# Kernel optimization log

Hardware: AMD Instinct MI355X
Metric: run time of the kernel (lower is better)

Reference implementation:

```python
import jax, jax.numpy as jnp
import numpy as np

N_NODES = 50000


def _gcn_layer(x, src, dst, norm_src, norm_dst, W, b, act):
    # DGL GraphConv with norm='both': D_out^{-1/2} A D_in^{-1/2} X W + b
    h = x * norm_src[:, None]                      # scale by src out-degree
    m = h[src]                                     # gather messages [E, d]
    agg = jax.ops.segment_sum(m, dst, num_segments=N_NODES)  # scatter-add
    agg = agg * norm_dst[:, None]
    out = agg @ W + b
    if act:
        out = jax.nn.relu(out)
    return out


def setup_inputs() -> dict:
    key = jax.random.key(0)
    ks = jax.random.split(key, 10)
    E = 800000
    in_size, hid, out_size = 128, 128, 64
    features = jax.random.normal(ks[0], (N_NODES, in_size), dtype=jnp.float32)
    src = jax.random.randint(ks[1], (E,), 0, N_NODES, dtype=jnp.int32)
    dst = jax.random.randint(ks[2], (E,), 0, N_NODES, dtype=jnp.int32)
    s = 0.05
    W1 = jax.random.normal(ks[3], (in_size, hid), dtype=jnp.float32) * s
    b1 = jnp.zeros((hid,), dtype=jnp.float32)
    W2 = jax.random.normal(ks[4], (hid, hid), dtype=jnp.float32) * s
    b2 = jnp.zeros((hid,), dtype=jnp.float32)
    W3 = jax.random.normal(ks[5], (hid, out_size), dtype=jnp.float32) * s
    b3 = jnp.zeros((out_size,), dtype=jnp.float32)
    return {"features": features, "W1": W1, "b1": b1, "W2": W2, "b2": b2,
            "W3": W3, "b3": b3, "src": src, "dst": dst}


def reference(features, W1, b1, W2, b2, W3, b3, src, dst):
    ones = jnp.ones(src.shape, dtype=features.dtype)
    out_deg = jax.ops.segment_sum(ones, src, num_segments=N_NODES)
    in_deg = jax.ops.segment_sum(ones, dst, num_segments=N_NODES)
    norm_src = jnp.maximum(out_deg, 1.0) ** -0.5   # clamp(min=1) as in DGL
    norm_dst = jnp.maximum(in_deg, 1.0) ** -0.5
    h = _gcn_layer(features, src, dst, norm_src, norm_dst, W1, b1, act=True)
    # dropout is identity in eval mode
    h = _gcn_layer(h, src, dst, norm_src, norm_dst, W2, b2, act=True)
    h = _gcn_layer(h, src, dst, norm_src, norm_dst, W3, b3, act=False)
    return h
```

## Files before the change

### kernel.cpp

```cpp
#include <hip/hip_runtime.h>
#include <math.h>

#define N_NODES 50000
#define K_DIM 128
#define CAP 64
#define CHUNK 25000
#define RH 25000
#define HWORDS 12500

typedef __attribute__((ext_vector_type(8))) short short8_t;
typedef __attribute__((ext_vector_type(4))) float f32x4_t;
typedef __attribute__((ext_vector_type(8))) _Float16 half8_t;

__device__ inline unsigned short f2bf(float x) {
    unsigned u = __float_as_uint(x);
    unsigned r = u + 0x7fffu + ((u >> 16) & 1u);
    return (unsigned short)(r >> 16);
}
__device__ inline float bf2f(unsigned short h) {
    return __uint_as_float(((unsigned)h) << 16);
}

__global__ void init_zero_kernel(_Float16* Yx, _Float16* Yy, _Float16* Yz) {
    int t = threadIdx.x;
    if (t < 128) {
        Yx[(size_t)N_NODES * 128 + t] = (_Float16)0.f;
        Yy[(size_t)N_NODES * 128 + t] = (_Float16)0.f;
    }
    if (t < 64) Yz[(size_t)N_NODES * 64 + t] = (_Float16)0.f;
}


__global__ __launch_bounds__(1024) void hist_kernel(const int* __restrict__ src,
                                                    const int* __restrict__ dst, int E,
                                                    unsigned* __restrict__ pin,
                                                    unsigned* __restrict__ pout) {
    __shared__ unsigned h[HWORDS];
    int b  = blockIdx.x >> 2;
    int io = (blockIdx.x >> 1) & 1;
    int r  = blockIdx.x & 1;
    int tid = threadIdx.x;
    for (int t = tid; t < HWORDS; t += 1024) h[t] = 0;
    __syncthreads();
    const int* keys = io ? src : dst;
    int start = b * CHUNK;
    int end = start + CHUNK; if (end > E) end = E;
    int vlo = r * RH;
    for (int i = start + tid; i < end; i += 1024) {
        int v = keys[i] - vlo;
        if ((unsigned)v < (unsigned)RH)
            atomicAdd(&h[v >> 1], 1u << ((v & 1) * 16));
    }
    __syncthreads();
    unsigned* out = io ? pout : pin;
    for (int t = tid; t < HWORDS; t += 1024)
        out[(size_t)b * (2 * HWORDS) + r * HWORDS + t] = h[t];
}

__global__ void offsets_norm_kernel(const unsigned* __restrict__ pin,
                                    const unsigned* __restrict__ pout,
                                    unsigned short* __restrict__ off16,
                                    int* __restrict__ indeg,
                                    float* __restrict__ nsrc, float* __restrict__ ndst,
                                    int n, int NB) {
    int v = blockIdx.x * blockDim.x + threadIdx.x;
    if (v >= n) return;
    int wi = v >> 1, sh = (v & 1) * 16;
    int od = 0;
    for (int b = 0; b < NB; ++b)
        od += (pout[(size_t)b * (2 * HWORDS) + wi] >> sh) & 0xffff;
    int run = 0;
    for (int b = 0; b < NB; ++b) {
        int c = (pin[(size_t)b * (2 * HWORDS) + wi] >> sh) & 0xffff;
        off16[(size_t)b * n + v] = (unsigned short)(run < CAP ? run : CAP);
        run += c;
    }
    indeg[v] = run < CAP ? run : CAP;
    int odc = od < 1 ? 1 : od;
    int idc = run < 1 ? 1 : run;
    nsrc[v] = 1.0f / sqrtf((float)odc);
    ndst[v] = 1.0f / sqrtf((float)idc);
}

__global__ __launch_bounds__(1024) void scatter_kernel(const int* __restrict__ src,
                                                       const int* __restrict__ dst, int E,
                                                       const unsigned short* __restrict__ off16,
                                                       int* __restrict__ csr, int n) {
    __shared__ unsigned cur[HWORDS];
    int b = blockIdx.x >> 1;
    int r = blockIdx.x & 1;
    int tid = threadIdx.x;
    int vlo = r * RH;
    const unsigned short* offb = off16 + (size_t)b * n + vlo;
    for (int t = tid; t < HWORDS; t += 1024)
        cur[t] = (unsigned)offb[2 * t] | ((unsigned)offb[2 * t + 1] << 16);
    __syncthreads();
    int start = b * CHUNK;
    int end = start + CHUNK; if (end > E) end = E;
    for (int i = start + tid; i < end; i += 1024) {
        int v = dst[i];
        int vr = v - vlo;
        if ((unsigned)vr < (unsigned)RH) {
            int sh = (vr & 1) * 16;
            unsigned old = atomicAdd(&cur[vr >> 1], 1u << sh);
            unsigned p = (old >> sh) & 0xffff;
            if (p < CAP) csr[((size_t)v << 6) + p] = src[i];
        }
    }
}

__global__ void split_w_all_kernel(const float* __restrict__ W1,
                                   const float* __restrict__ W2,
                                   const float* __restrict__ W3,
                                   unsigned short* __restrict__ W1h, unsigned short* __restrict__ W1l,
                                   unsigned short* __restrict__ W2h, unsigned short* __restrict__ W2l,
                                   unsigned short* __restrict__ W3h, unsigned short* __restrict__ W3l) {
    int gi = blockIdx.x * blockDim.x + threadIdx.x;
    const float* W; unsigned short *WBh, *WBl; int M, i;
    if (gi < 2048)      { W = W1; WBh = W1h; WBl = W1l; M = 128; i = gi; }
    else if (gi < 4096) { W = W2; WBh = W2h; WBl = W2l; M = 128; i = gi - 2048; }
    else if (gi < 5120) { W = W3; WBh = W3h; WBl = W3l; M = 64;  i = gi - 4096; }
    else return;
    int c    = i >> 8;
    int rem  = i & 255;
    int kc   = rem >> 6;
    int lane = rem & 63;
    int m = lane & 15, q = lane >> 4;
    int n = c * 16 + m;
    #pragma unroll
    for (int j = 0; j < 8; ++j) {
        int k = kc * 32 + q * 8 + j;
        float w = W[(size_t)k * M + n];
        unsigned short hi = f2bf(w);
        unsigned short lo = f2bf(w - bf2f(hi));
        WBh[(size_t)i * 8 + j] = hi;
        WBl[(size_t)i * 8 + j] = lo;
    }
}

template <int M>
__global__ __launch_bounds__(256) void gemm_mfma_kernel(
        const float* __restrict__ X,
        const unsigned short* __restrict__ WBh_,
        const unsigned short* __restrict__ WBl_,
        const float* __restrict__ nsrc, _Float16* __restrict__ Yh, int n) {
    constexpr int LSTR = 136;
    __shared__ short Xhi[64 * LSTR];
    __shared__ short Xlo[64 * LSTR];
    int tid = threadIdx.x;
    int lane = tid & 63, wave = tid >> 6;
    int rowBlock = blockIdx.x * 64;

    #pragma unroll
    for (int l = 0; l < 8; ++l) {
        int idx = (tid + l * 256) * 4;
        int r = idx >> 7;
        int c = idx & 127;
        float4 v = make_float4(0.f, 0.f, 0.f, 0.f);
        int gr = rowBlock + r;
        if (gr < n) v = *(const float4*)&X[(size_t)gr * K_DIM + c];
        unsigned short h0 = f2bf(v.x), h1 = f2bf(v.y), h2 = f2bf(v.z), h3 = f2bf(v.w);
        short4 hs = {(short)h0, (short)h1, (short)h2, (short)h3};
        short4 ls = {(short)f2bf(v.x - bf2f(h0)), (short)f2bf(v.y - bf2f(h1)),
                     (short)f2bf(v.z - bf2f(h2)), (short)f2bf(v.w - bf2f(h3))};
        *(short4*)&Xhi[r * LSTR + c] = hs;
        *(short4*)&Xlo[r * LSTR + c] = ls;
    }
    __syncthreads();

    int m = lane & 15, q = lane >> 4;
    short8_t ah[4], al[4];
    {
        int abase = (wave * 16 + m) * LSTR + q * 8;
        #pragma unroll
        for (int kc = 0; kc < 4; ++kc) {
            ah[kc] = *(const short8_t*)&Xhi[abase + kc * 32];
            al[kc] = *(const short8_t*)&Xlo[abase + kc * 32];
        }
    }
    float ns[4];
    int orow0 = rowBlock + wave * 16 + q * 4;
    #pragma unroll
    for (int r = 0; r < 4; ++r) ns[r] = (orow0 + r < n) ? nsrc[orow0 + r] : 0.f;

    const short8_t* WBh = (const short8_t*)WBh_;
    const short8_t* WBl = (const short8_t*)WBl_;
    constexpr int CT = M / 16;
    #pragma unroll
    for (int c = 0; c < CT; ++c) {
        short8_t bh[4], bl[4];
        #pragma unroll
        for (int kc = 0; kc < 4; ++kc) {
            bh[kc] = WBh[(c * 4 + kc) * 64 + lane];
            bl[kc] = WBl[(c * 4 + kc) * 64 + lane];
        }
        f32x4_t acc = {0.f, 0.f, 0.f, 0.f};
        #pragma unroll
        for (int kc = 0; kc < 4; ++kc) {
            acc = __builtin_amdgcn_mfma_f32_16x16x32_bf16(ah[kc], bh[kc], acc, 0, 0, 0);
            acc = __builtin_amdgcn_mfma_f32_16x16x32_bf16(ah[kc], bl[kc], acc, 0, 0, 0);
            acc = __builtin_amdgcn_mfma_f32_16x16x32_bf16(al[kc], bh[kc], acc, 0, 0, 0);
        }
        int col = c * 16 + m;
        #pragma unroll
        for (int r = 0; r < 4; ++r) {
            int row = orow0 + r;
            if (row < n) Yh[(size_t)row * M + col] = (_Float16)(acc[r] * ns[r]);
        }
    }
}

template <int MOUT>
__global__ __launch_bounds__(256) void agg_gemm_kernel(
        const _Float16* __restrict__ Yin,
        const int* __restrict__ indeg, const int* __restrict__ csr,
        const float* __restrict__ ndst, const float* __restrict__ bias,
        const unsigned short* __restrict__ WBh_,
        const unsigned short* __restrict__ WBl_,
        const float* __restrict__ nsrc, _Float16* __restrict__ Yout, int n) {
    constexpr int LSTR = 136;
    __shared__ short Xhi[32 * LSTR];
    __shared__ short Xlo[32 * LSTR];
    int tid = threadIdx.x;
    int lane = tid & 63, wave = tid >> 6;
    int rowBlock = blockIdx.x * 32;

    int sub = tid >> 4;
    int f8  = (tid & 15) * 8;
    #pragma unroll
    for (int p = 0; p < 2; ++p) {
        int r = p * 16 + sub;
        int v = rowBlock + r;
        float o[8] = {};
        if (v < n) {
            int deg = indeg[v];
            const int* __restrict__ row = &csr[(size_t)v * CAP];
            float acc[8] = {};
            for (int i = 0; i < deg; i += 8) {
                int4 sa = *(const int4*)&row[i];
                int4 sb = *(const int4*)&row[i + 4];
                int s0 = sa.x;
                int s1 = (i + 1 < deg) ? sa.y : N_NODES;
                int s2 = (i + 2 < deg) ? sa.z : N_NODES;
                int s3 = (i + 3 < deg) ? sa.w : N_NODES;
                int s4 = (i + 4 < deg) ? sb.x : N_NODES;
                int s5 = (i + 5 < deg) ? sb.y : N_NODES;
                int s6 = (i + 6 < deg) ? sb.z : N_NODES;
                int s7 = (i + 7 < deg) ? sb.w : N_NODES;
                half8_t a = *(const half8_t*)&Yin[(size_t)s0 * 128 + f8];
                half8_t b = *(const half8_t*)&Yin[(size_t)s1 * 128 + f8];
                half8_t c = *(const half8_t*)&Yin[(size_t)s2 * 128 + f8];
                half8_t d = *(const half8_t*)&Yin[(size_t)s3 * 128 + f8];
                half8_t e = *(const half8_t*)&Yin[(size_t)s4 * 128 + f8];
                half8_t f = *(const half8_t*)&Yin[(size_t)s5 * 128 + f8];
                half8_t g = *(const half8_t*)&Yin[(size_t)s6 * 128 + f8];
                half8_t h = *(const half8_t*)&Yin[(size_t)s7 * 128 + f8];
                #pragma unroll
                for (int j = 0; j < 8; ++j)
                    acc[j] += (((float)a[j] + (float)b[j]) + ((float)c[j] + (float)d[j]))
                            + (((float)e[j] + (float)f[j]) + ((float)g[j] + (float)h[j]));
            }
            float nd = ndst[v];
            #pragma unroll
            for (int j = 0; j < 8; ++j)
                o[j] = fmaxf(nd * acc[j] + bias[f8 + j], 0.f);
        }
        short hs[8], ls[8];
        #pragma unroll
        for (int j = 0; j < 8; ++j) {
            unsigned short h = f2bf(o[j]);
            hs[j] = (short)h;
            ls[j] = (short)f2bf(o[j] - bf2f(h));
        }
        *(short4*)&Xhi[r * LSTR + f8]     = *(short4*)&hs[0];
        *(short4*)&Xhi[r * LSTR + f8 + 4] = *(short4*)&hs[4];
        *(short4*)&Xlo[r * LSTR + f8]     = *(short4*)&ls[0];
        *(short4*)&Xlo[r * LSTR + f8 + 4] = *(short4*)&ls[4];
    }
    __syncthreads();

    int m = lane & 15, q = lane >> 4;
    int wrow = wave & 1;
    int wcol = wave >> 1;
    short8_t ah[4], al[4];
    {
        int abase = (wrow * 16 + m) * LSTR + q * 8;
        #pragma unroll
        for (int kc = 0; kc < 4; ++kc) {
            ah[kc] = *(const short8_t*)&Xhi[abase + kc * 32];
            al[kc] = *(const short8_t*)&Xlo[abase + kc * 32];
        }
    }
    float ns[4];
    int orow0 = rowBlock + wrow * 16 + q * 4;
    #pragma unroll
    for (int r = 0; r < 4; ++r) ns[r] = (orow0 + r < n) ? nsrc[orow0 + r] : 0.f;

    const short8_t* WBh = (const short8_t*)WBh_;
    const short8_t* WBl = (const short8_t*)WBl_;
    constexpr int CTH = MOUT / 32;
    #pragma unroll
    for (int c2 = 0; c2 < CTH; ++c2) {
        int c = wcol * CTH + c2;
        short8_t bh[4], bl[4];
        #pragma unroll
        for (int kc = 0; kc < 4; ++kc) {
            bh[kc] = WBh[(c * 4 + kc) * 64 + lane];
            bl[kc] = WBl[(c * 4 + kc) * 64 + lane];
        }
        f32x4_t acc = {0.f, 0.f, 0.f, 0.f};
        #pragma unroll
        for (int kc = 0; kc < 4; ++kc) {
            acc = __builtin_amdgcn_mfma_f32_16x16x32_bf16(ah[kc], bh[kc], acc, 0, 0, 0);
            acc = __builtin_amdgcn_mfma_f32_16x16x32_bf16(ah[kc], bl[kc], acc, 0, 0, 0);
            acc = __builtin_amdgcn_mfma_f32_16x16x32_bf16(al[kc], bh[kc], acc, 0, 0, 0);
        }
        int col = c * 16 + m;
        #pragma unroll
        for (int r = 0; r < 4; ++r) {
            int row = orow0 + r;
            if (row < n) Yout[(size_t)row * MOUT + col] = (_Float16)(acc[r] * ns[r]);
        }
    }
}

template <int M, bool RELU>
__global__ __launch_bounds__(256) void agg_kernel(const _Float16* __restrict__ Y,
                                                  const int* __restrict__ indeg,
                                                  const int* __restrict__ csr,
                                                  const float* __restrict__ ndst,
                                                  const float* __restrict__ bias,
                                                  float* __restrict__ Z, int n) {
    constexpr int LPN = M / 8;
    constexpr int NPB = 256 / LPN;
    int v = blockIdx.x * NPB + threadIdx.x / LPN;
    if (v >= n) return;
    int f8 = (threadIdx.x % LPN) * 8;
    int deg = indeg[v];
    const int* __restrict__ row = &csr[(size_t)v * CAP];
    float acc[8] = {};
    for (int i = 0; i < deg; i += 8) {
        int4 sa = *(const int4*)&row[i];
        int4 sb = *(const int4*)&row[i + 4];
        int s0 = sa.x;
        int s1 = (i + 1 < deg) ? sa.y : N_NODES;
        int s2 = (i + 2 < deg) ? sa.z : N_NODES;
        int s3 = (i + 3 < deg) ? sa.w : N_NODES;
        int s4 = (i + 4 < deg) ? sb.x : N_NODES;
        int s5 = (i + 5 < deg) ? sb.y : N_NODES;
        int s6 = (i + 6 < deg) ? sb.z : N_NODES;
        int s7 = (i + 7 < deg) ? sb.w : N_NODES;
        half8_t a = *(const half8_t*)&Y[(size_t)s0 * M + f8];
        half8_t b = *(const half8_t*)&Y[(size_t)s1 * M + f8];
        half8_t c = *(const half8_t*)&Y[(size_t)s2 * M + f8];
        half8_t d = *(const half8_t*)&Y[(size_t)s3 * M + f8];
        half8_t e = *(const half8_t*)&Y[(size_t)s4 * M + f8];
        half8_t f = *(const half8_t*)&Y[(size_t)s5 * M + f8];
        half8_t g = *(const half8_t*)&Y[(size_t)s6 * M + f8];
        half8_t h = *(const half8_t*)&Y[(size_t)s7 * M + f8];
        #pragma unroll
        for (int j = 0; j < 8; ++j)
            acc[j] += (((float)a[j] + (float)b[j]) + ((float)c[j] + (float)d[j]))
                    + (((float)e[j] + (float)f[j]) + ((float)g[j] + (float)h[j]));
    }
    float nd = ndst[v];
    float4 bb0 = *(const float4*)&bias[f8];
    float4 bb1 = *(const float4*)&bias[f8 + 4];
    float o[8];
    o[0] = nd * acc[0] + bb0.x; o[1] = nd * acc[1] + bb0.y;
    o[2] = nd * acc[2] + bb0.z; o[3] = nd * acc[3] + bb0.w;
    o[4] = nd * acc[4] + bb1.x; o[5] = nd * acc[5] + bb1.y;
    o[6] = nd * acc[6] + bb1.z; o[7] = nd * acc[7] + bb1.w;
    if (RELU) {
        #pragma unroll
        for (int j = 0; j < 8; ++j) o[j] = fmaxf(o[j], 0.f);
    }
    *(float4*)&Z[(size_t)v * M + f8]     = make_float4(o[0], o[1], o[2], o[3]);
    *(float4*)&Z[(size_t)v * M + f8 + 4] = make_float4(o[4], o[5], o[6], o[7]);
}


extern "C" void kernel_launch(void* const* d_in, const int* in_sizes, int n_in,
                              void* d_out, int out_size, void* d_ws, size_t ws_size,
                              hipStream_t stream) {
    const float* features = (const float*)d_in[0];
    const float* W1 = (const float*)d_in[1];
    const float* b1 = (const float*)d_in[2];
    const float* W2 = (const float*)d_in[3];
    const float* b2 = (const float*)d_in[4];
    const float* W3 = (const float*)d_in[5];
    const float* b3 = (const float*)d_in[6];
    const int* src = (const int*)d_in[7];
    const int* dst = (const int*)d_in[8];
    const int E = in_sizes[7];
    const int N = N_NODES;
    const int NB = (E + CHUNK - 1) / CHUNK;

    char* w = (char*)d_ws;
    auto alloc = [&](size_t bytes) {
        char* p = w;
        w += (bytes + 255) & ~(size_t)255;
        return p;
    };
    _Float16* Yx = (_Float16*)alloc((size_t)(N + 1) * 128 * 2);
    _Float16* Yy = (_Float16*)alloc((size_t)(N + 1) * 128 * 2);
    _Float16* Yz = (_Float16*)alloc((size_t)(N + 1) * 64 * 2);
    int*   csr    = (int*)alloc((size_t)N * CAP * 4);
    unsigned* pin  = (unsigned*)alloc((size_t)NB * 2 * HWORDS * 4);
    unsigned* pout = (unsigned*)alloc((size_t)NB * 2 * HWORDS * 4);
    unsigned short* off16 = (unsigned short*)alloc((size_t)NB * N * 2);
    int*   indeg  = (int*)alloc((size_t)N * 4);
    float* nsrc   = (float*)alloc((size_t)N * 4);
    float* ndst   = (float*)alloc((size_t)N * 4);
    unsigned short* W1h = (unsigned short*)alloc(128 * 128 * 2);
    unsigned short* W1l = (unsigned short*)alloc(128 * 128 * 2);
    unsigned short* W2h = (unsigned short*)alloc(128 * 128 * 2);
    unsigned short* W2l = (unsigned short*)alloc(128 * 128 * 2);
    unsigned short* W3h = (unsigned short*)alloc(64 * 128 * 2);
    unsigned short* W3l = (unsigned short*)alloc(64 * 128 * 2);

    init_zero_kernel<<<1, 128, 0, stream>>>(Yx, Yy, Yz);
    hist_kernel<<<NB * 4, 1024, 0, stream>>>(src, dst, E, pin, pout);
    offsets_norm_kernel<<<(N + 255) / 256, 256, 0, stream>>>(pin, pout, off16, indeg,
                                                             nsrc, ndst, N, NB);
    scatter_kernel<<<NB * 2, 1024, 0, stream>>>(src, dst, E, off16, csr, N);
    split_w_all_kernel<<<20, 256, 0, stream>>>(W1, W2, W3, W1h, W1l, W2h, W2l, W3h, W3l);

    int gblocks64 = (N + 63) / 64;
    int gblocks32 = (N + 31) / 32;
    gemm_mfma_kernel<128><<<gblocks64, 256, 0, stream>>>(features, W1h, W1l, nsrc, Yx, N);
    agg_gemm_kernel<128><<<gblocks32, 256, 0, stream>>>(Yx, indeg, csr, ndst, b1,
                                                        W2h, W2l, nsrc, Yy, N);
    agg_gemm_kernel<64><<<gblocks32, 256, 0, stream>>>(Yy, indeg, csr, ndst, b2,
                                                       W3h, W3l, nsrc, Yz, N);
    agg_kernel<64, false><<<(N + 31) / 32, 256, 0, stream>>>(Yz, indeg, csr, ndst, b3,
                                                             (float*)d_out, N);
}
```

Measured before the change: 240.2 us.

## Store fp16 feature matrices in 32-column chunks to shrink gather working set

```diff
diff --git a/kernel.cpp b/kernel.cpp
--- a/kernel.cpp
+++ b/kernel.cpp
@@ -8,9 +8,12 @@
 #define RH 25000
 #define HWORDS 12500
 
+#define CSP ((size_t)(N_NODES + 1) * 32)
+
 typedef __attribute__((ext_vector_type(8))) short short8_t;
 typedef __attribute__((ext_vector_type(4))) float f32x4_t;
 typedef __attribute__((ext_vector_type(8))) _Float16 half8_t;
+typedef __attribute__((ext_vector_type(4))) _Float16 half4_t;
 
 __device__ inline unsigned short f2bf(float x) {
     unsigned u = __float_as_uint(x);
@@ -23,11 +26,10 @@
 
 __global__ void init_zero_kernel(_Float16* Yx, _Float16* Yy, _Float16* Yz) {
     int t = threadIdx.x;
-    if (t < 128) {
-        Yx[(size_t)N_NODES * 128 + t] = (_Float16)0.f;
-        Yy[(size_t)N_NODES * 128 + t] = (_Float16)0.f;
-    }
-    if (t < 64) Yz[(size_t)N_NODES * 64 + t] = (_Float16)0.f;
+    int c = t >> 5, f = t & 31;
+    Yx[c * CSP + (size_t)N_NODES * 32 + f] = (_Float16)0.f;
+    Yy[c * CSP + (size_t)N_NODES * 32 + f] = (_Float16)0.f;
+    if (c < 2) Yz[c * CSP + (size_t)N_NODES * 32 + f] = (_Float16)0.f;
 }
 
 
@@ -202,10 +204,12 @@
             acc = __builtin_amdgcn_mfma_f32_16x16x32_bf16(al[kc], bh[kc], acc, 0, 0, 0);
         }
         int col = c * 16 + m;
+        int ch = col >> 5, cc = col & 31;
         #pragma unroll
         for (int r = 0; r < 4; ++r) {
             int row = orow0 + r;
-            if (row < n) Yh[(size_t)row * M + col] = (_Float16)(acc[r] * ns[r]);
+            if (row < n)
+                Yh[(size_t)ch * CSP + (size_t)row * 32 + cc] = (_Float16)(acc[r] * ns[r]);
         }
     }
 }
@@ -225,17 +229,17 @@
     int lane = tid & 63, wave = tid >> 6;
     int rowBlock = blockIdx.x * 32;
 
-    int sub = tid >> 4;
-    int f8  = (tid & 15) * 8;
-    #pragma unroll
-    for (int p = 0; p < 2; ++p) {
-        int r = p * 16 + sub;
+    {
+        int r  = tid >> 3;
+        int f4 = (tid & 7) * 4;
         int v = rowBlock + r;
-        float o[8] = {};
-        if (v < n) {
-            int deg = indeg[v];
-            const int* __restrict__ row = &csr[(size_t)v * CAP];
-            float acc[8] = {};
+        int deg = 0; float nd = 0.f;
+        const int* __restrict__ row = &csr[(size_t)v * CAP];
+        if (v < n) { deg = indeg[v]; nd = ndst[v]; }
+        #pragma unroll 1
+        for (int cch = 0; cch < 4; ++cch) {
+            const _Float16* __restrict__ base = Yin + (size_t)cch * CSP + f4;
+            float acc[4] = {};
             for (int i = 0; i < deg; i += 8) {
                 int4 sa = *(const int4*)&row[i];
                 int4 sb = *(const int4*)&row[i + 4];
@@ -247,35 +251,35 @@
                 int s5 = (i + 5 < deg) ? sb.y : N_NODES;
                 int s6 = (i + 6 < deg) ? sb.z : N_NODES;
                 int s7 = (i + 7 < deg) ? sb.w : N_NODES;
-                half8_t a = *(const half8_t*)&Yin[(size_t)s0 * 128 + f8];
-                half8_t b = *(const half8_t*)&Yin[(size_t)s1 * 128 + f8];
-                half8_t c = *(const half8_t*)&Yin[(size_t)s2 * 128 + f8];
-                half8_t d = *(const half8_t*)&Yin[(size_t)s3 * 128 + f8];
-                half8_t e = *(const half8_t*)&Yin[(size_t)s4 * 128 + f8];
-                half8_t f = *(const half8_t*)&Yin[(size_t)s5 * 128 + f8];
-                half8_t g = *(const half8_t*)&Yin[(size_t)s6 * 128 + f8];
-                half8_t h = *(const half8_t*)&Yin[(size_t)s7 * 128 + f8];
+                half4_t a = *(const half4_t*)&base[(size_t)s0 * 32];
+                half4_t b = *(const half4_t*)&base[(size_t)s1 * 32];
+                half4_t c = *(const half4_t*)&base[(size_t)s2 * 32];
+                half4_t d = *(const half4_t*)&base[(size_t)s3 * 32];
+                half4_t e = *(const half4_t*)&base[(size_t)s4 * 32];
+                half4_t f = *(const half4_t*)&base[(size_t)s5 * 32];
+                half4_t g = *(const half4_t*)&base[(size_t)s6 * 32];
+                half4_t h = *(const half4_t*)&base[(size_t)s7 * 32];
                 #pragma unroll
-                for (int j = 0; j < 8; ++j)
-                    acc[j] += (((float)a[j] + (float)b[j]) + ((float)c[j] + (float)d[j]))
-                            + (((float)e[j] + (float)f[j]) + ((float)g[j] + (float)h[j]));
+                for (int t = 0; t < 4; ++t)
+                    acc[t] += (((float)a[t] + (float)b[t]) + ((float)c[t] + (float)d[t]))
+                            + (((float)e[t] + (float)f[t]) + ((float)g[t] + (float)h[t]));
             }
-            float nd = ndst[v];
+            float o[4] = {};
+            if (v < n) {
+                #pragma unroll
+                for (int t = 0; t < 4; ++t)
+                    o[t] = fmaxf(nd * acc[t] + bias[cch * 32 + f4 + t], 0.f);
+            }
+            short hs[4], ls[4];
             #pragma unroll
-            for (int j = 0; j < 8; ++j)
-                o[j] = fmaxf(nd * acc[j] + bias[f8 + j], 0.f);
-        }
-        short hs[8], ls[8];
-        #pragma unroll
-        for (int j = 0; j < 8; ++j) {
-            unsigned short h = f2bf(o[j]);
-            hs[j] = (short)h;
-            ls[j] = (short)f2bf(o[j] - bf2f(h));
-        }
-        *(short4*)&Xhi[r * LSTR + f8]     = *(short4*)&hs[0];
-        *(short4*)&Xhi[r * LSTR + f8 + 4] = *(short4*)&hs[4];
-        *(short4*)&Xlo[r * LSTR + f8]     = *(short4*)&ls[0];
-        *(short4*)&Xlo[r * LSTR + f8 + 4] = *(short4*)&ls[4];
+            for (int t = 0; t < 4; ++t) {
+                unsigned short h = f2bf(o[t]);
+                hs[t] = (short)h;
+                ls[t] = (short)f2bf(o[t] - bf2f(h));
+            }
+            *(short4*)&Xhi[r * LSTR + cch * 32 + f4] = *(short4*)&hs[0];
+            *(short4*)&Xlo[r * LSTR + cch * 32 + f4] = *(short4*)&ls[0];
+        }
     }
     __syncthreads();
 
@@ -316,67 +320,65 @@
             acc = __builtin_amdgcn_mfma_f32_16x16x32_bf16(al[kc], bh[kc], acc, 0, 0, 0);
         }
         int col = c * 16 + m;
+        int ch = col >> 5, cc = col & 31;
         #pragma unroll
         for (int r = 0; r < 4; ++r) {
             int row = orow0 + r;
-            if (row < n) Yout[(size_t)row * MOUT + col] = (_Float16)(acc[r] * ns[r]);
-        }
-    }
-}
-
-template <int M, bool RELU>
-__global__ __launch_bounds__(256) void agg_kernel(const _Float16* __restrict__ Y,
-                                                  const int* __restrict__ indeg,
-                                                  const int* __restrict__ csr,
-                                                  const float* __restrict__ ndst,
-                                                  const float* __restrict__ bias,
-                                                  float* __restrict__ Z, int n) {
-    constexpr int LPN = M / 8;
-    constexpr int NPB = 256 / LPN;
-    int v = blockIdx.x * NPB + threadIdx.x / LPN;
+            if (row < n)
+                Yout[(size_t)ch * CSP + (size_t)row * 32 + cc] = (_Float16)(acc[r] * ns[r]);
+        }
+    }
+}
+
+__global__ __launch_bounds__(256) void agg_final_kernel(const _Float16* __restrict__ Y,
+                                                        const int* __restrict__ indeg,
+                                                        const int* __restrict__ csr,
+                                                        const float* __restrict__ ndst,
+                                                        const float* __restrict__ bias,
+                                                        float* __restrict__ Z, int n) {
+    int r  = threadIdx.x >> 3;
+    int f4 = (threadIdx.x & 7) * 4;
+    int v = blockIdx.x * 32 + r;
     if (v >= n) return;
-    int f8 = (threadIdx.x % LPN) * 8;
     int deg = indeg[v];
+    float nd = ndst[v];
     const int* __restrict__ row = &csr[(size_t)v * CAP];
-    float acc[8] = {};
-    for (int i = 0; i < deg; i += 8) {
-        int4 sa = *(const int4*)&row[i];
-        int4 sb = *(const int4*)&row[i + 4];
-        int s0 = sa.x;
-        int s1 = (i + 1 < deg) ? sa.y : N_NODES;
-        int s2 = (i + 2 < deg) ? sa.z : N_NODES;
-        int s3 = (i + 3 < deg) ? sa.w : N_NODES;
-        int s4 = (i + 4 < deg) ? sb.x : N_NODES;
-        int s5 = (i + 5 < deg) ? sb.y : N_NODES;
-        int s6 = (i + 6 < deg) ? sb.z : N_NODES;
-        int s7 = (i + 7 < deg) ? sb.w : N_NODES;
-        half8_t a = *(const half8_t*)&Y[(size_t)s0 * M + f8];
-        half8_t b = *(const half8_t*)&Y[(size_t)s1 * M + f8];
-        half8_t c = *(const half8_t*)&Y[(size_t)s2 * M + f8];
-        half8_t d = *(const half8_t*)&Y[(size_t)s3 * M + f8];
-        half8_t e = *(const half8_t*)&Y[(size_t)s4 * M + f8];
-        half8_t f = *(const half8_t*)&Y[(size_t)s5 * M + f8];
-        half8_t g = *(const half8_t*)&Y[(size_t)s6 * M + f8];
-        half8_t h = *(const half8_t*)&Y[(size_t)s7 * M + f8];
-        #pragma unroll
-        for (int j = 0; j < 8; ++j)
-            acc[j] += (((float)a[j] + (float)b[j]) + ((float)c[j] + (float)d[j]))
-                    + (((float)e[j] + (float)f[j]) + ((float)g[j] + (float)h[j]));
-    }
-    float nd = ndst[v];
-    float4 bb0 = *(const float4*)&bias[f8];
-    float4 bb1 = *(const float4*)&bias[f8 + 4];
-    float o[8];
-    o[0] = nd * acc[0] + bb0.x; o[1] = nd * acc[1] + bb0.y;
-    o[2] = nd * acc[2] + bb0.z; o[3] = nd * acc[3] + bb0.w;
-    o[4] = nd * acc[4] + bb1.x; o[5] = nd * acc[5] + bb1.y;
-    o[6] = nd * acc[6] + bb1.z; o[7] = nd * acc[7] + bb1.w;
-    if (RELU) {
-        #pragma unroll
-        for (int j = 0; j < 8; ++j) o[j] = fmaxf(o[j], 0.f);
-    }
-    *(float4*)&Z[(size_t)v * M + f8]     = make_float4(o[0], o[1], o[2], o[3]);
-    *(float4*)&Z[(size_t)v * M + f8 + 4] = make_float4(o[4], o[5], o[6], o[7]);
+    #pragma unroll 1
+    for (int c = 0; c < 2; ++c) {
+        const _Float16* __restrict__ base = Y + (size_t)c * CSP + f4;
+        float acc[4] = {};
+        for (int i = 0; i < deg; i += 8) {
+            int4 sa = *(const int4*)&row[i];
+            int4 sb = *(const int4*)&row[i + 4];
+            int s0 = sa.x;
+            int s1 = (i + 1 < deg) ? sa.y : N_NODES;
+            int s2 = (i + 2 < deg) ? sa.z : N_NODES;
+            int s3 = (i + 3 < deg) ? sa.w : N_NODES;
+            int s4 = (i + 4 < deg) ? sb.x : N_NODES;
+            int s5 = (i + 5 < deg) ? sb.y : N_NODES;
+            int s6 = (i + 6 < deg) ? sb.z : N_NODES;
+            int s7 = (i + 7 < deg) ? sb.w : N_NODES;
+            half4_t a = *(const half4_t*)&base[(size_t)s0 * 32];
+            half4_t b = *(const half4_t*)&base[(size_t)s1 * 32];
+            half4_t c2 = *(const half4_t*)&base[(size_t)s2 * 32];
+            half4_t d = *(const half4_t*)&base[(size_t)s3 * 32];
+            half4_t e = *(const half4_t*)&base[(size_t)s4 * 32];
+            half4_t f = *(const half4_t*)&base[(size_t)s5 * 32];
+            half4_t g = *(const half4_t*)&base[(size_t)s6 * 32];
+            half4_t h = *(const half4_t*)&base[(size_t)s7 * 32];
+            #pragma unroll
+            for (int t = 0; t < 4; ++t)
+                acc[t] += (((float)a[t] + (float)b[t]) + ((float)c2[t] + (float)d[t]))
+                        + (((float)e[t] + (float)f[t]) + ((float)g[t] + (float)h[t]));
+        }
+        int fbase = c * 32 + f4;
+        float4 bb = *(const float4*)&bias[fbase];
+        float o0 = nd * acc[0] + bb.x;
+        float o1 = nd * acc[1] + bb.y;
+        float o2 = nd * acc[2] + bb.z;
+        float o3 = nd * acc[3] + bb.w;
+        *(float4*)&Z[(size_t)v * 64 + fbase] = make_float4(o0, o1, o2, o3);
+    }
 }
 
 
@@ -433,6 +435,6 @@
                                                         W2h, W2l, nsrc, Yy, N);
     agg_gemm_kernel<64><<<gblocks32, 256, 0, stream>>>(Yy, indeg, csr, ndst, b2,
                                                        W3h, W3l, nsrc, Yz, N);
-    agg_kernel<64, false><<<(N + 31) / 32, 256, 0, stream>>>(Yz, indeg, csr, ndst, b3,
-                                                             (float*)d_out, N);
-}
+    agg_final_kernel<<<gblocks32, 256, 0, stream>>>(Yz, indeg, csr, ndst, b3,
+                                                    (float*)d_out, N);
+}
```

Result: slower. 269.5 us (+12.2%).
